# Optimization experiments

Measured on AMD Instinct MI355X. Metric: run time of the kernel, lower is better.

Reference implementation:

```python
import jax, jax.numpy as jnp
import numpy as np

N_NODES = 5000
N_EDGES = 50000
HIDDEN = 64
EDGE_DIM = 16


def setup_inputs() -> dict:
    key = jax.random.key(0)
    ks = jax.random.split(key, 8)
    d = HIDDEN
    h = jax.random.normal(ks[0], (N_NODES, d), dtype=jnp.float32)
    edge_index = jax.random.randint(ks[1], (2, N_EDGES), 0, N_NODES, dtype=jnp.int64)
    edge_features = jax.random.normal(ks[2], (N_EDGES, EDGE_DIM), dtype=jnp.float32)
    # edge-network MLP: Linear(edge_dim, d) -> ReLU -> Linear(d, d*d)
    W1 = jax.random.normal(ks[3], (EDGE_DIM, d), dtype=jnp.float32) * (1.0 / np.sqrt(EDGE_DIM))
    b1 = jnp.zeros((d,), dtype=jnp.float32)
    W2 = jax.random.normal(ks[4], (d, d * d), dtype=jnp.float32) * (1.0 / np.sqrt(d))
    b2 = jnp.zeros((d * d,), dtype=jnp.float32)
    # GRUCell params (torch layout: rows = [reset; update; new])
    W_ih = jax.random.normal(ks[5], (3 * d, d), dtype=jnp.float32) * (1.0 / np.sqrt(d))
    W_hh = jax.random.normal(ks[6], (3 * d, d), dtype=jnp.float32) * (1.0 / np.sqrt(d))
    b_ih = jnp.zeros((3 * d,), dtype=jnp.float32)
    b_hh = jnp.zeros((3 * d,), dtype=jnp.float32)
    return {"h": h, "edge_index": edge_index, "edge_features": edge_features,
            "W1": W1, "b1": b1, "W2": W2, "b2": b2,
            "W_ih": W_ih, "W_hh": W_hh, "b_ih": b_ih, "b_hh": b_hh}


def reference(h, edge_index, edge_features, W1, b1, W2, b2, W_ih, W_hh, b_ih, b_hh):
    n_nodes, d = h.shape
    src, tgt = edge_index[0], edge_index[1]
    # 1) gather sender states
    h_w = h[src]  # (E, d)
    # 2-3) edge MLP -> per-edge transformation matrices (E, d, d)
    A = jax.nn.relu(edge_features @ W1 + b1) @ W2 + b2
    A = A.reshape(-1, d, d)
    # 4) per-edge matvec messages
    msg = jnp.einsum('eij,ej->ei', A, h_w)  # (E, d)
    # 5) scatter-sum aggregation per target node
    m = jax.ops.segment_sum(msg, tgt, num_segments=n_nodes)  # (N, d)
    # 6) GRUCell(m, h) - torch semantics
    gi = m @ W_ih.T + b_ih   # (N, 3d)
    gh = h @ W_hh.T + b_hh   # (N, 3d)
    i_r, i_z, i_n = jnp.split(gi, 3, axis=-1)
    h_r, h_z, h_n = jnp.split(gh, 3, axis=-1)
    r = jax.nn.sigmoid(i_r + h_r)
    z = jax.nn.sigmoid(i_z + h_z)
    n = jnp.tanh(i_n + r * h_n)
    h_new = (1.0 - z) * n + z * h
    return h_new
```

## Files before the change

kernel.cpp:

```cpp
#include <hip/hip_runtime.h>
#include <math.h>

#define N_NODES 5000
#define N_EDGES 50000
#define NPAD 5024
#define KP 4224
#define KSPLIT 3
#define POISON_I ((int)0xAAAAAAAAu)

typedef _Float16 f16x8 __attribute__((ext_vector_type(8)));
typedef _Float16 f16x2 __attribute__((ext_vector_type(2)));
typedef float    f32x4 __attribute__((ext_vector_type(4)));

static __device__ __forceinline__ f32x4 mfma16f(f16x8 a, f16x8 b, f32x4 c) {
    return __builtin_amdgcn_mfma_f32_16x16x32_f16(a, b, c, 0, 0, 0);
}

__global__ void prep_kernel(const float* __restrict__ W2, const float* __restrict__ b2,
                            const float* __restrict__ Wih, const float* __restrict__ Whh,
                            const int* __restrict__ ei,
                            _Float16* __restrict__ Br, _Float16* __restrict__ Bg2,
                            int* __restrict__ cnt) {
    int g = blockIdx.x * 256 + threadIdx.x;
    if (g < 33792) {
        int nt = g / 8448, rem = g - nt * 8448;
        int ks = rem >> 6, lane = rem & 63;
        int lo = lane & 15, q = lane >> 4;
        int i = nt * 16 + lo, kap0 = ks * 32 + q * 8;
        f16x8 v;
#pragma unroll
        for (int p = 0; p < 8; ++p) {
            int kap = kap0 + p;
            int k2 = kap >> 7, rem2 = kap & 127;
            int j = rem2 >> 1, k = k2 * 2 + (rem2 & 1);
            float x = 0.f;
            if (k < 64) x = W2[(size_t)k * 4096 + i * 64 + j];
            else if (k == 64) x = b2[i * 64 + j];
            v[p] = (_Float16)x;
        }
        *(f16x8*)(Br + (size_t)g * 8) = v;
        return;
    }
    g -= 33792;
    if (g < 3072) {
        int ct = g >> 7, ks = (g >> 6) & 1, lane = g & 63;
        int lo = lane & 15, q = lane >> 4;
        const float* src = (ct < 12) ? Wih : Whh;
        int r = ((ct < 12) ? ct : ct - 12) * 16 + lo;
        int j0 = ks * 32 + q * 8;
        f16x8 v;
#pragma unroll
        for (int p = 0; p < 8; ++p) v[p] = (_Float16)src[r * 64 + j0 + p];
        *(f16x8*)(Bg2 + (size_t)g * 8) = v;
        return;
    }
    g -= 3072;
    if (g < N_EDGES) atomicAdd(&cnt[ei[N_EDGES + g]], 1);
}

__global__ __launch_bounds__(1024) void scan_kernel(const int* __restrict__ cnt,
                                                    int* __restrict__ off,
                                                    int* __restrict__ cur) {
    __shared__ int s[1024];
    int tid = threadIdx.x;
    int base = tid * 5;
    int loc[5]; int sum = 0;
#pragma unroll
    for (int q = 0; q < 5; ++q) {
        int v = (base + q < N_NODES) ? (cnt[base + q] - POISON_I) : 0;
        loc[q] = sum; sum += v;
    }
    s[tid] = sum; __syncthreads();
    for (int d = 1; d < 1024; d <<= 1) {
        int v = (tid >= d) ? s[tid - d] : 0;
        __syncthreads();
        s[tid] += v;
        __syncthreads();
    }
    int excl = (tid > 0) ? s[tid - 1] : 0;
#pragma unroll
    for (int q = 0; q < 5; ++q)
        if (base + q < N_NODES) { off[base + q] = excl + loc[q]; cur[base + q] = excl + loc[q]; }
    if (tid == 1023) off[N_NODES] = excl + sum;
}

__global__ void scatter_kernel(const int* __restrict__ ei, int* __restrict__ cur,
                               int* __restrict__ srcp, int* __restrict__ eidp) {
    int e = blockIdx.x * 256 + threadIdx.x;
    if (e < N_EDGES) {
        int q = atomicAdd(&cur[ei[N_EDGES + e]], 1);
        srcp[q] = ei[e];
        eidp[q] = e;
    }
}

__global__ __launch_bounds__(256) void hbuild_kernel(const int* __restrict__ toff,
                                                     const int* __restrict__ srcp,
                                                     const int* __restrict__ eidp,
                                                     const float* __restrict__ ef,
                                                     const float* __restrict__ W1,
                                                     const float* __restrict__ b1,
                                                     const float* __restrict__ h,
                                                     _Float16* __restrict__ H) {
    __shared__ _Float16 tls[16][64];
    __shared__ float hls[16][64];
    int tid = threadIdx.x, kc = tid >> 6, lane = tid & 63;
    int v = blockIdx.x;
    float acc[16];
#pragma unroll
    for (int k = 0; k < 16; ++k) acc[k] = 0.f;
    float acc64 = 0.f;
    int s0 = 0, s1 = 0;
    if (v < N_NODES) { s0 = toff[v]; s1 = toff[v + 1]; }
    float w1c[16];
#pragma unroll
    for (int k = 0; k < 16; ++k) w1c[k] = W1[k * 64 + lane];
    float b1l = b1[lane];
    for (int tb = s0; tb < s1; tb += 16) {
        int tcnt = s1 - tb; if (tcnt > 16) tcnt = 16;
        int eidx[4], sidx[4];
#pragma unroll
        for (int r = 0; r < 4; ++r) {
            int idx = kc * 4 + r;
            if (idx < tcnt) {
                eidx[r] = eidp[tb + idx];
                sidx[r] = srcp[tb + idx];
            }
        }
#pragma unroll
        for (int r = 0; r < 4; ++r) {
            int idx = kc * 4 + r;
            if (idx < tcnt) {
                hls[idx][lane] = h[(size_t)sidx[r] * 64 + lane];
                const float* efr = ef + (size_t)eidx[r] * 16;
                float tacc = b1l;
#pragma unroll
                for (int k = 0; k < 16; ++k) tacc += efr[k] * w1c[k];
                tls[idx][lane] = (_Float16)fmaxf(tacc, 0.f);
            }
        }
        __syncthreads();
        int q = 0;
        for (; q + 1 < tcnt; q += 2) {
            float hv0 = hls[q][lane];
            float hv1 = hls[q + 1][lane];
            const f16x8* t0 = (const f16x8*)&tls[q][kc * 16];
            const f16x8* t1 = (const f16x8*)&tls[q + 1][kc * 16];
            f16x8 a0 = t0[0], a1 = t0[1];
            f16x8 c0 = t1[0], c1 = t1[1];
#pragma unroll
            for (int p = 0; p < 8; ++p) {
                acc[p]     += (float)a0[p] * hv0 + (float)c0[p] * hv1;
                acc[8 + p] += (float)a1[p] * hv0 + (float)c1[p] * hv1;
            }
            acc64 += hv0 + hv1;
        }
        if (q < tcnt) {
            float hv = hls[q][lane];
            const f16x8* t0 = (const f16x8*)&tls[q][kc * 16];
            f16x8 a0 = t0[0], a1 = t0[1];
#pragma unroll
            for (int p = 0; p < 8; ++p) {
                acc[p]     += (float)a0[p] * hv;
                acc[8 + p] += (float)a1[p] * hv;
            }
            acc64 += hv;
        }
        __syncthreads();
    }
    _Float16* Hv = H + (size_t)v * KP;
#pragma unroll
    for (int p = 0; p < 8; ++p) {
        f16x2 pv = { (_Float16)acc[p * 2], (_Float16)acc[p * 2 + 1] };
        *(f16x2*)(Hv + (kc * 8 + p) * 128 + lane * 2) = pv;
    }
    if (kc == 3) {
        f16x2 pv = { (_Float16)acc64, (_Float16)0.f };
        *(f16x2*)(Hv + 32 * 128 + lane * 2) = pv;
    }
}

__global__ __launch_bounds__(256) void gemm_part(const _Float16* __restrict__ H,
                                                 const _Float16* __restrict__ Br,
                                                 float* __restrict__ gp) {
    __shared__ _Float16 As[2][32 * 136];
    int tid = threadIdx.x, w = tid >> 6, lane = tid & 63;
    int lo = lane & 15, q = lane >> 4;
    int m0 = blockIdx.x * 32;
    int ksp = blockIdx.y;
    int ar = tid >> 4, ac = (tid & 15) * 8;
    const _Float16* Ag0 = H + (size_t)(m0 + ar) * KP + ksp * 1408 + ac;
    const _Float16* Ag1 = Ag0 + (size_t)16 * KP;
    f32x4 acc0 = {0.f, 0.f, 0.f, 0.f}, acc1 = acc0;
    f16x8 pf0 = *(const f16x8*)(Ag0);
    f16x8 pf1 = *(const f16x8*)(Ag1);
    *(f16x8*)(&As[0][ar * 136 + ac]) = pf0;
    *(f16x8*)(&As[0][(ar + 16) * 136 + ac]) = pf1;
    __syncthreads();
    for (int c = 0; c < 11; ++c) {
        if (c + 1 < 11) {
            pf0 = *(const f16x8*)(Ag0 + (size_t)(c + 1) * 128);
            pf1 = *(const f16x8*)(Ag1 + (size_t)(c + 1) * 128);
        }
        const _Float16* Abuf = &As[c & 1][0];
        int ksg = (ksp * 11 + c) * 4;
#pragma unroll
        for (int ks = 0; ks < 4; ++ks) {
            f16x8 b = *(const f16x8*)(Br + ((size_t)((w * 132 + ksg + ks) * 64 + lane)) * 8);
            f16x8 a0 = *(const f16x8*)(Abuf + lo * 136 + ks * 32 + q * 8);
            f16x8 a1 = *(const f16x8*)(Abuf + (16 + lo) * 136 + ks * 32 + q * 8);
            acc0 = mfma16f(a0, b, acc0);
            acc1 = mfma16f(a1, b, acc1);
        }
        if (c + 1 < 11) {
            *(f16x8*)(&As[(c + 1) & 1][ar * 136 + ac]) = pf0;
            *(f16x8*)(&As[(c + 1) & 1][(ar + 16) * 136 + ac]) = pf1;
        }
        __syncthreads();
    }
    float* gpo = gp + (size_t)ksp * NPAD * 64;
    int row4 = q * 4;
#pragma unroll
    for (int g = 0; g < 4; ++g) {
        gpo[(size_t)(m0 + row4 + g) * 64 + w * 16 + lo]      = acc0[g];
        gpo[(size_t)(m0 + 16 + row4 + g) * 64 + w * 16 + lo] = acc1[g];
    }
}

__global__ __launch_bounds__(256) void gru_mfma(const float* __restrict__ gp,
                                                const float* __restrict__ h,
                                                const _Float16* __restrict__ Bg2,
                                                const float* __restrict__ bih,
                                                const float* __restrict__ bhh,
                                                float* __restrict__ out) {
    __shared__ _Float16 mls[16 * 72];
    __shared__ _Float16 hls[16 * 72];
    __shared__ float gbuf[16 * 385];
    int tid = threadIdx.x, w = tid >> 6, lane = tid & 63;
    int lo = lane & 15, q = lane >> 4;
    int m0 = blockIdx.x * 16;
#pragma unroll
    for (int r = 0; r < 4; ++r) {
        int idx = r * 256 + tid, nl = idx >> 6, j = idx & 63;
        int n = m0 + nl;
        float mv = 0.f, hv = 0.f;
        if (n < N_NODES) {
            size_t o = (size_t)n * 64 + j;
            mv = gp[o] + gp[(size_t)NPAD * 64 + o] + gp[(size_t)2 * NPAD * 64 + o];
            hv = h[o];
        }
        mls[nl * 72 + j] = (_Float16)mv;
        hls[nl * 72 + j] = (_Float16)hv;
    }
    __syncthreads();
    f16x8 am[2], ah[2];
    am[0] = *(const f16x8*)&mls[lo * 72 + q * 8];
    am[1] = *(const f16x8*)&mls[lo * 72 + 32 + q * 8];
    ah[0] = *(const f16x8*)&hls[lo * 72 + q * 8];
    ah[1] = *(const f16x8*)&hls[lo * 72 + 32 + q * 8];
    f32x4 zero4 = {0.f, 0.f, 0.f, 0.f};
    f32x4 acc[6] = {zero4, zero4, zero4, zero4, zero4, zero4};
#pragma unroll
    for (int j = 0; j < 3; ++j) {
        int ctg = w + 4 * j;
        int cth = 12 + w + 4 * j;
#pragma unroll
        for (int ks = 0; ks < 2; ++ks) {
            f16x8 bg = *(const f16x8*)(Bg2 + ((size_t)((ctg * 2 + ks) * 64 + lane)) * 8);
            f16x8 bh = *(const f16x8*)(Bg2 + ((size_t)((cth * 2 + ks) * 64 + lane)) * 8);
            acc[j]     = mfma16f(am[ks], bg, acc[j]);
            acc[3 + j] = mfma16f(ah[ks], bh, acc[3 + j]);
        }
    }
#pragma unroll
    for (int j = 0; j < 3; ++j) {
        int colg = (w + 4 * j) * 16 + lo;
        int colh = 192 + colg;
#pragma unroll
        for (int g = 0; g < 4; ++g) {
            gbuf[(q * 4 + g) * 385 + colg] = acc[j][g];
            gbuf[(q * 4 + g) * 385 + colh] = acc[3 + j][g];
        }
    }
    __syncthreads();
    int i = lane;
#pragma unroll
    for (int u = 0; u < 4; ++u) {
        int nl = w * 4 + u, n = m0 + nl;
        if (n >= N_NODES) continue;
        const float* gb = gbuf + nl * 385;
        float ir  = gb[i]       + bih[i];
        float iz  = gb[64 + i]  + bih[64 + i];
        float inn = gb[128 + i] + bih[128 + i];
        float hr  = gb[192 + i] + bhh[i];
        float hz  = gb[256 + i] + bhh[64 + i];
        float hn  = gb[320 + i] + bhh[128 + i];
        float hval = h[(size_t)n * 64 + i];
        float r = 1.f / (1.f + expf(-(ir + hr)));
        float z = 1.f / (1.f + expf(-(iz + hz)));
        float nn = tanhf(inn + r * hn);
        out[n * 64 + i] = (1.f - z) * nn + z * hval;
    }
}

extern "C" void kernel_launch(void* const* d_in, const int* in_sizes, int n_in,
                              void* d_out, int out_size, void* d_ws, size_t ws_size,
                              hipStream_t stream) {
    const float* h   = (const float*)d_in[0];
    const int*   ei  = (const int*)d_in[1];
    const float* ef  = (const float*)d_in[2];
    const float* W1  = (const float*)d_in[3];
    const float* b1  = (const float*)d_in[4];
    const float* W2  = (const float*)d_in[5];
    const float* b2  = (const float*)d_in[6];
    const float* Wih = (const float*)d_in[7];
    const float* Whh = (const float*)d_in[8];
    const float* bih = (const float*)d_in[9];
    const float* bhh = (const float*)d_in[10];
    float* out = (float*)d_out;

    _Float16* H    = (_Float16*)d_ws;
    _Float16* Br   = H + (size_t)NPAD * KP;
    _Float16* Bg2  = Br + 270336;
    float*    gp   = (float*)(Bg2 + 24576);
    int*      cnt  = (int*)(gp + (size_t)KSPLIT * NPAD * 64);
    int*      toff = cnt + N_NODES;
    int*      cur  = toff + N_NODES + 1;
    int*      srcp = cur + N_NODES;
    int*      eidp = srcp + N_EDGES;

    prep_kernel<<<340, 256, 0, stream>>>(W2, b2, Wih, Whh, ei, Br, Bg2, cnt);
    scan_kernel<<<1, 1024, 0, stream>>>(cnt, toff, cur);
    scatter_kernel<<<196, 256, 0, stream>>>(ei, cur, srcp, eidp);
    hbuild_kernel<<<NPAD, 256, 0, stream>>>(toff, srcp, eidp, ef, W1, b1, h, H);
    gemm_part<<<dim3(157, KSPLIT), 256, 0, stream>>>(H, Br, gp);
    gru_mfma<<<314, 256, 0, stream>>>(gp, h, Bg2, bih, bhh, out);
}
```

Before: 134.2 us.

## Fuse split-K message GEMM with GRU kernel, splitting K across warps in-block

Merges the split-K GEMM (which wrote three fp32 partial buffers to global memory) and the GRU kernel into one 512-thread kernel over 16-node tiles. The K reduction is split between two warp halves and combined through shared memory instead of global partials. This removes one kernel launch and the global partial-sum round trip. The cost is a serial 33-step K loop per block with a sync each step, and 314 blocks where there were 471 GEMM blocks, so parallelism and latency hiding may drop.

```diff
diff --git a/kernel.cpp b/kernel.cpp
--- a/kernel.cpp
+++ b/kernel.cpp
@@ -5,7 +5,6 @@
 #define N_EDGES 50000
 #define NPAD 5024
 #define KP 4224
-#define KSPLIT 3
 #define POISON_I ((int)0xAAAAAAAAu)
 
 typedef _Float16 f16x8 __attribute__((ext_vector_type(8)));
@@ -180,113 +179,100 @@
     }
 }
 
-__global__ __launch_bounds__(256) void gemm_part(const _Float16* __restrict__ H,
-                                                 const _Float16* __restrict__ Br,
-                                                 float* __restrict__ gp) {
-    __shared__ _Float16 As[2][32 * 136];
-    int tid = threadIdx.x, w = tid >> 6, lane = tid & 63;
-    int lo = lane & 15, q = lane >> 4;
-    int m0 = blockIdx.x * 32;
-    int ksp = blockIdx.y;
-    int ar = tid >> 4, ac = (tid & 15) * 8;
-    const _Float16* Ag0 = H + (size_t)(m0 + ar) * KP + ksp * 1408 + ac;
-    const _Float16* Ag1 = Ag0 + (size_t)16 * KP;
-    f32x4 acc0 = {0.f, 0.f, 0.f, 0.f}, acc1 = acc0;
-    f16x8 pf0 = *(const f16x8*)(Ag0);
-    f16x8 pf1 = *(const f16x8*)(Ag1);
-    *(f16x8*)(&As[0][ar * 136 + ac]) = pf0;
-    *(f16x8*)(&As[0][(ar + 16) * 136 + ac]) = pf1;
-    __syncthreads();
-    for (int c = 0; c < 11; ++c) {
-        if (c + 1 < 11) {
-            pf0 = *(const f16x8*)(Ag0 + (size_t)(c + 1) * 128);
-            pf1 = *(const f16x8*)(Ag1 + (size_t)(c + 1) * 128);
-        }
-        const _Float16* Abuf = &As[c & 1][0];
-        int ksg = (ksp * 11 + c) * 4;
-#pragma unroll
-        for (int ks = 0; ks < 4; ++ks) {
-            f16x8 b = *(const f16x8*)(Br + ((size_t)((w * 132 + ksg + ks) * 64 + lane)) * 8);
-            f16x8 a0 = *(const f16x8*)(Abuf + lo * 136 + ks * 32 + q * 8);
-            f16x8 a1 = *(const f16x8*)(Abuf + (16 + lo) * 136 + ks * 32 + q * 8);
-            acc0 = mfma16f(a0, b, acc0);
-            acc1 = mfma16f(a1, b, acc1);
-        }
-        if (c + 1 < 11) {
-            *(f16x8*)(&As[(c + 1) & 1][ar * 136 + ac]) = pf0;
-            *(f16x8*)(&As[(c + 1) & 1][(ar + 16) * 136 + ac]) = pf1;
-        }
-        __syncthreads();
-    }
-    float* gpo = gp + (size_t)ksp * NPAD * 64;
-    int row4 = q * 4;
-#pragma unroll
-    for (int g = 0; g < 4; ++g) {
-        gpo[(size_t)(m0 + row4 + g) * 64 + w * 16 + lo]      = acc0[g];
-        gpo[(size_t)(m0 + 16 + row4 + g) * 64 + w * 16 + lo] = acc1[g];
-    }
-}
-
-__global__ __launch_bounds__(256) void gru_mfma(const float* __restrict__ gp,
+__global__ __launch_bounds__(512) void gemm_gru(const _Float16* __restrict__ H,
+                                                const _Float16* __restrict__ Br,
+                                                const _Float16* __restrict__ Bg2,
                                                 const float* __restrict__ h,
-                                                const _Float16* __restrict__ Bg2,
                                                 const float* __restrict__ bih,
                                                 const float* __restrict__ bhh,
                                                 float* __restrict__ out) {
+    __shared__ _Float16 As[2][16 * 136];
+    __shared__ float    mbuf[16][65];
     __shared__ _Float16 mls[16 * 72];
     __shared__ _Float16 hls[16 * 72];
-    __shared__ float gbuf[16 * 385];
-    int tid = threadIdx.x, w = tid >> 6, lane = tid & 63;
+    __shared__ float    gbuf[16 * 385];
+    int tid = threadIdx.x, w8 = tid >> 6, lane = tid & 63;
     int lo = lane & 15, q = lane >> 4;
+    int nt = w8 & 3, kh = w8 >> 2;
     int m0 = blockIdx.x * 16;
-#pragma unroll
-    for (int r = 0; r < 4; ++r) {
-        int idx = r * 256 + tid, nl = idx >> 6, j = idx & 63;
-        int n = m0 + nl;
-        float mv = 0.f, hv = 0.f;
-        if (n < N_NODES) {
-            size_t o = (size_t)n * 64 + j;
-            mv = gp[o] + gp[(size_t)NPAD * 64 + o] + gp[(size_t)2 * NPAD * 64 + o];
-            hv = h[o];
-        }
-        mls[nl * 72 + j] = (_Float16)mv;
-        hls[nl * 72 + j] = (_Float16)hv;
-    }
+    int ar = tid >> 4, ac = (tid & 15) * 8;
+    const _Float16* Ag = H + (size_t)(m0 + ar) * KP + ac;
+    const f16x8* BrV = (const f16x8*)Br;
+    f32x4 acc = {0.f, 0.f, 0.f, 0.f};
+    if (tid < 256)
+        *(f16x8*)(&As[0][ar * 136 + ac]) = *(const f16x8*)(Ag);
+    f16x8 b0 = BrV[((size_t)(nt * 132 + kh * 2 + 0)) * 64 + lane];
+    f16x8 b1 = BrV[((size_t)(nt * 132 + kh * 2 + 1)) * 64 + lane];
     __syncthreads();
-    f16x8 am[2], ah[2];
-    am[0] = *(const f16x8*)&mls[lo * 72 + q * 8];
-    am[1] = *(const f16x8*)&mls[lo * 72 + 32 + q * 8];
-    ah[0] = *(const f16x8*)&hls[lo * 72 + q * 8];
-    ah[1] = *(const f16x8*)&hls[lo * 72 + 32 + q * 8];
-    f32x4 zero4 = {0.f, 0.f, 0.f, 0.f};
-    f32x4 acc[6] = {zero4, zero4, zero4, zero4, zero4, zero4};
+    for (int c = 0; c < 33; ++c) {
+        f16x8 pf, nb0, nb1;
+        if (tid < 256 && c + 1 < 33)
+            pf = *(const f16x8*)(Ag + (size_t)(c + 1) * 128);
+        if (c + 1 < 33) {
+            nb0 = BrV[((size_t)(nt * 132 + (c + 1) * 4 + kh * 2 + 0)) * 64 + lane];
+            nb1 = BrV[((size_t)(nt * 132 + (c + 1) * 4 + kh * 2 + 1)) * 64 + lane];
+        }
+        const _Float16* Ab = &As[c & 1][0];
+        f16x8 a0 = *(const f16x8*)(Ab + lo * 136 + (kh * 2 + 0) * 32 + q * 8);
+        f16x8 a1 = *(const f16x8*)(Ab + lo * 136 + (kh * 2 + 1) * 32 + q * 8);
+        acc = mfma16f(a0, b0, acc);
+        acc = mfma16f(a1, b1, acc);
+        if (tid < 256 && c + 1 < 33)
+            *(f16x8*)(&As[(c + 1) & 1][ar * 136 + ac]) = pf;
+        __syncthreads();
+        b0 = nb0; b1 = nb1;
+    }
+    if (kh == 1) {
+#pragma unroll
+        for (int g = 0; g < 4; ++g) mbuf[q * 4 + g][nt * 16 + lo] = acc[g];
+    }
+    __syncthreads();
+    if (kh == 0) {
+#pragma unroll
+        for (int g = 0; g < 4; ++g) {
+            float mv = acc[g] + mbuf[q * 4 + g][nt * 16 + lo];
+            mls[(q * 4 + g) * 72 + nt * 16 + lo] = (_Float16)mv;
+        }
+    } else {
+        int t2 = (w8 - 4) * 64 + lane;
+#pragma unroll
+        for (int r = 0; r < 4; ++r) {
+            int e = r * 256 + t2, nl = e >> 6, j = e & 63;
+            int n = m0 + nl;
+            float hv = (n < N_NODES) ? h[(size_t)n * 64 + j] : 0.f;
+            hls[nl * 72 + j] = (_Float16)hv;
+        }
+    }
+    __syncthreads();
+    f16x8 am0 = *(const f16x8*)&mls[lo * 72 + q * 8];
+    f16x8 am1 = *(const f16x8*)&mls[lo * 72 + 32 + q * 8];
+    f16x8 ah0 = *(const f16x8*)&hls[lo * 72 + q * 8];
+    f16x8 ah1 = *(const f16x8*)&hls[lo * 72 + 32 + q * 8];
+    const f16x8* BgV = (const f16x8*)Bg2;
+    f32x4 z4 = {0.f, 0.f, 0.f, 0.f};
+    f32x4 ga[3] = {z4, z4, z4};
 #pragma unroll
     for (int j = 0; j < 3; ++j) {
-        int ctg = w + 4 * j;
-        int cth = 12 + w + 4 * j;
-#pragma unroll
-        for (int ks = 0; ks < 2; ++ks) {
-            f16x8 bg = *(const f16x8*)(Bg2 + ((size_t)((ctg * 2 + ks) * 64 + lane)) * 8);
-            f16x8 bh = *(const f16x8*)(Bg2 + ((size_t)((cth * 2 + ks) * 64 + lane)) * 8);
-            acc[j]     = mfma16f(am[ks], bg, acc[j]);
-            acc[3 + j] = mfma16f(ah[ks], bh, acc[3 + j]);
-        }
+        int ct = w8 + 8 * j;
+        f16x8 bg0 = BgV[((size_t)(ct * 2 + 0)) * 64 + lane];
+        f16x8 bg1 = BgV[((size_t)(ct * 2 + 1)) * 64 + lane];
+        f16x8 a0f = (ct < 12) ? am0 : ah0;
+        f16x8 a1f = (ct < 12) ? am1 : ah1;
+        ga[j] = mfma16f(a0f, bg0, ga[j]);
+        ga[j] = mfma16f(a1f, bg1, ga[j]);
     }
 #pragma unroll
     for (int j = 0; j < 3; ++j) {
-        int colg = (w + 4 * j) * 16 + lo;
-        int colh = 192 + colg;
-#pragma unroll
-        for (int g = 0; g < 4; ++g) {
-            gbuf[(q * 4 + g) * 385 + colg] = acc[j][g];
-            gbuf[(q * 4 + g) * 385 + colh] = acc[3 + j][g];
-        }
+        int ct = w8 + 8 * j;
+        int col = (ct < 12) ? (ct * 16 + lo) : (192 + (ct - 12) * 16 + lo);
+#pragma unroll
+        for (int g = 0; g < 4; ++g) gbuf[(q * 4 + g) * 385 + col] = ga[j][g];
     }
     __syncthreads();
     int i = lane;
 #pragma unroll
-    for (int u = 0; u < 4; ++u) {
-        int nl = w * 4 + u, n = m0 + nl;
+    for (int u = 0; u < 2; ++u) {
+        int nl = w8 * 2 + u, n = m0 + nl;
         if (n >= N_NODES) continue;
         const float* gb = gbuf + nl * 385;
         float ir  = gb[i]       + bih[i];
@@ -322,8 +308,7 @@
     _Float16* H    = (_Float16*)d_ws;
     _Float16* Br   = H + (size_t)NPAD * KP;
     _Float16* Bg2  = Br + 270336;
-    float*    gp   = (float*)(Bg2 + 24576);
-    int*      cnt  = (int*)(gp + (size_t)KSPLIT * NPAD * 64);
+    int*      cnt  = (int*)(Bg2 + 24576);
     int*      toff = cnt + N_NODES;
     int*      cur  = toff + N_NODES + 1;
     int*      srcp = cur + N_NODES;
@@ -333,6 +318,5 @@
     scan_kernel<<<1, 1024, 0, stream>>>(cnt, toff, cur);
     scatter_kernel<<<196, 256, 0, stream>>>(ei, cur, srcp, eidp);
     hbuild_kernel<<<NPAD, 256, 0, stream>>>(toff, srcp, eidp, ef, W1, b1, h, H);
-    gemm_part<<<dim3(157, KSPLIT), 256, 0, stream>>>(H, Br, gp);
-    gru_mfma<<<314, 256, 0, stream>>>(gp, h, Bg2, bih, bhh, out);
-}
+    gemm_gru<<<314, 512, 0, stream>>>(H, Br, Bg2, h, bih, bhh, out);
+}
```

Measured after the change: 135.8 us. About the same (+1.1%).
